# Kernel tuning notes

Measured on AMD Instinct MI355X. Metric: run time of the kernel, lower is better.

## Reference

```python
import jax, jax.numpy as jnp
import numpy as np

THETA = 10000.0
BLOCK_SIZE = 8192  # max_cache_len; T >= BLOCK_SIZE triggers eviction
NEG_INF = -1e30


def _rope_cos_sin(head_dim, seq_len, dtype):
    inv_freq = 1.0 / (THETA ** (jnp.arange(0, head_dim, 2, dtype=jnp.float32) / head_dim))
    freqs = jnp.arange(seq_len, dtype=jnp.float32)[:, None] * inv_freq[None, :]  # (T, hd/2)
    return jnp.cos(freqs).astype(dtype), jnp.sin(freqs).astype(dtype)


def _apply_rope(x, cos, sin):
    # x: (B, T, hd); complex multiply on interleaved pairs, matching torch.view_as_complex
    B, T, hd = x.shape
    xr = x.reshape(B, T, hd // 2, 2)
    x0, x1 = xr[..., 0], xr[..., 1]
    out = jnp.stack([x0 * cos - x1 * sin, x0 * sin + x1 * cos], axis=-1)
    return out.reshape(B, T, hd)


def setup_inputs() -> dict:
    key = jax.random.key(0)
    kx, kk, kq, kv = jax.random.split(key, 4)
    B, T, C, hd = 1, 8192, 1024, 64
    x = jax.random.normal(kx, (B, T, C), dtype=jnp.float32)
    Wk = 0.02 * jax.random.normal(kk, (C, hd), dtype=jnp.float32)
    Wq = 0.02 * jax.random.normal(kq, (C, hd), dtype=jnp.float32)
    Wv = 0.02 * jax.random.normal(kv, (C, hd), dtype=jnp.float32)
    return {"x": x, "Wk": Wk, "Wq": Wq, "Wv": Wv}


def reference(x, Wk, Wq, Wv):
    # Warm-up branch of Head.forward: RoPE QK causal attention + importance-based eviction.
    B, T, C = x.shape
    hd = Wk.shape[1]
    k = x @ Wk  # (B, T, hd)
    q = x @ Wq
    v = x @ Wv
    cos, sin = _rope_cos_sin(hd, T, x.dtype)
    k = _apply_rope(k, cos, sin)
    q = _apply_rope(q, cos, sin)
    scale = hd ** -0.5
    scores = jnp.einsum('btd,bsd->bts', q, k) * scale  # (B, T, T)
    causal = jnp.tril(jnp.ones((T, T), dtype=bool))
    scores = jnp.where(causal[None], scores, NEG_INF)
    wei = jax.nn.softmax(scores, axis=-1)
    out = jnp.einsum('bts,bsd->btd', wei, v)  # (B, T, hd)
    # importance-based KV-cache eviction (T >= BLOCK_SIZE here)
    col_sums = wei.sum(axis=1)  # (B, T)
    evict_id = jnp.argmin(col_sums.reshape(-1))  # flattened argmin, as torch.argmin (B=1)
    keep = jnp.arange(T - 1)
    keep = keep + (keep >= evict_id)  # all indices except evict_id
    importance = jnp.take(wei, keep, axis=1)  # evict row in dim 1: (B, T-1, T)
    cache_k = jnp.take(k, keep, axis=1)       # (B, T-1, hd)
    cache_v = jnp.take(v, keep, axis=1)       # (B, T-1, hd)
    return out, importance, cache_k, cache_v
```

## Files before the change

### kernel.cpp

```cpp
#include <hip/hip_runtime.h>

#define TT 8192
#define CC 1024
#define HD 64
#define TAIL0 (TT - 64)
#define IMP_OFF ((size_t)TT * HD)
#define CK_OFF (IMP_OFF + (size_t)(TT - 1) * TT)
#define CV_OFF (CK_OFF + (size_t)(TT - 1) * HD)

typedef float f32x4 __attribute__((ext_vector_type(4)));
typedef short short8 __attribute__((ext_vector_type(8)));

static __device__ __forceinline__ short f2bf(float f) {
  union { float f; unsigned u; } v; v.f = f;
  unsigned u = v.u;
  unsigned r = (u + 0x7fffu + ((u >> 16) & 1u)) >> 16;
  return (short)r;
}
static __device__ __forceinline__ float bf2f(short h) {
  union { unsigned u; float f; } v;
  v.u = ((unsigned)(unsigned short)h) << 16;
  return v.f;
}
static __device__ __forceinline__ f32x4 mfma16(short8 a, short8 b, f32x4 c) {
  return __builtin_amdgcn_mfma_f32_16x16x32_bf16(a, b, c, 0, 0, 0);
}
static __device__ __forceinline__ void nt_store4(float* p, f32x4 v) {
  __builtin_nontemporal_store(v, (f32x4*)p);
}

__global__ void prep(const float* __restrict__ Wk, const float* __restrict__ Wq,
                     const float* __restrict__ Wv, short* __restrict__ wth,
                     short* __restrict__ wtl, float* __restrict__ colsums,
                     float* __restrict__ ctab, float* __restrict__ stab) {
  const int b = blockIdx.x;
  if (b < 768) {
    const int tid = b * 256 + threadIdx.x;
    const int col = tid >> 10, c = tid & 1023;
    const int m = col >> 6, d = col & 63;
    const float* W = (m == 0) ? Wk : (m == 1) ? Wq : Wv;
    const float w = W[c * HD + d];
    const short h = f2bf(w);
    wth[col * CC + c] = h;
    wtl[col * CC + c] = f2bf(w - bf2f(h));
  } else if (b < 800) {
    const int t = (b - 768) * 256 + threadIdx.x;
    colsums[t] = 0.0f;
  } else {
    const int t = (b - 800) * 256 + threadIdx.x;
    const int row = t >> 5, fi = t & 31;
    const float inv = (float)(1.0 / pow(10000.0, (double)fi / 32.0));
    const float ang = (float)row * inv;
    float sn, cs;
    sincosf(ang, &sn, &cs);
    ctab[t] = cs; stab[t] = sn;
  }
}

__global__ __launch_bounds__(256) void qkv_rope(
    const float* __restrict__ x, const short* __restrict__ wth,
    const short* __restrict__ wtl, const float* __restrict__ ctab,
    const float* __restrict__ stab,
    short* __restrict__ qb, short* __restrict__ kb, short* __restrict__ vt,
    float* __restrict__ kf, float* __restrict__ vf, float* __restrict__ qf) {
  __shared__ short xsh[16][1024];
  __shared__ short xsl[16][1024];
  const int tid = threadIdx.x;
  const int lane = tid & 63, wv = tid >> 6;
  const int g = lane >> 4, lr = lane & 15, g8 = g * 8;
  const int r0 = blockIdx.x * 16;

  for (int i = tid; i < 16 * 128; i += 256) {
    const int row = i >> 7, u = i & 127;
    const float4 a4 = *(const float4*)&x[(size_t)(r0 + row) * CC + u * 8];
    const float4 b4 = *(const float4*)&x[(size_t)(r0 + row) * CC + u * 8 + 4];
    const float xv[8] = {a4.x, a4.y, a4.z, a4.w, b4.x, b4.y, b4.z, b4.w};
    short8 h, l;
#pragma unroll
    for (int t = 0; t < 8; ++t) {
      h[t] = f2bf(xv[t]);
      l[t] = f2bf(xv[t] - bf2f(h[t]));
    }
    const int us = (u ^ (row & 7)) * 8;
    *(short8*)&xsh[row][us] = h;
    *(short8*)&xsl[row][us] = l;
  }
  __syncthreads();

  const int ct0 = wv * 3;
  f32x4 acc[3];
#pragma unroll
  for (int i = 0; i < 3; ++i) acc[i] = (f32x4){0.f, 0.f, 0.f, 0.f};
  for (int kc = 0; kc < 32; ++kc) {
    const int us = ((kc * 4 + g) ^ (lr & 7)) * 8;
    const short8 ah = *(const short8*)&xsh[lr][us];
    const short8 al = *(const short8*)&xsl[lr][us];
    const int k0 = kc * 32 + g8;
#pragma unroll
    for (int t = 0; t < 3; ++t) {
      const int ct = ct0 + t;
      const short8 bh = *(const short8*)&wth[(ct * 16 + lr) * CC + k0];
      const short8 bl = *(const short8*)&wtl[(ct * 16 + lr) * CC + k0];
      acc[t] = mfma16(ah, bh, acc[t]);
      acc[t] = mfma16(al, bh, acc[t]);
      acc[t] = mfma16(ah, bl, acc[t]);
    }
  }
#pragma unroll
  for (int t = 0; t < 3; ++t) {
    const int col = ct0 * 16 + t * 16 + lr;
    const int m = col >> 6, d = col & 63;
#pragma unroll
    for (int r = 0; r < 4; ++r) {
      const int row = r0 + g * 4 + r;
      const float val = acc[t][r];
      if (m == 2) {
        vf[row * HD + d] = val;
        vt[(size_t)d * TT + row] = f2bf(val);
      } else {
        const float partner = __shfl_xor(val, 1);
        const int fi = d >> 1;
        const float cs = ctab[row * 32 + fi];
        const float sn = stab[row * 32 + fi];
        const float res = (d & 1) ? (partner * sn + val * cs)
                                  : (val * cs - partner * sn);
        if (m == 0) { kf[row * HD + d] = res; kb[row * HD + d] = f2bf(res); }
        else        { qf[row * HD + d] = res; qb[row * HD + d] = f2bf(res); }
      }
    }
  }
}

__global__ __launch_bounds__(512) void attn_row(
    const short* __restrict__ qb, const short* __restrict__ kb,
    const short* __restrict__ vt, float* __restrict__ colsums,
    float* __restrict__ outp, float* __restrict__ stash,
    float* __restrict__ linv_g) {
  const int tid = threadIdx.x;
  const int lane = tid & 63, wv = tid >> 6;
  const int g = lane >> 4, lr = lane & 15, g8 = g * 8;
  const int bid = (int)blockIdx.x;
  const int rt = (bid < 256) ? (511 - bid) : (bid - 256);
  const int r0 = rt * 16, rmax = r0 + 15;
  const int nkt = rt + 1;
  const int nktp = (nkt + 1) >> 1;
  float* imp = outp + IMP_OFF;
  const f32x4 z4 = (f32x4){0.f, 0.f, 0.f, 0.f};

  __shared__ float et[8][16][36];
  __shared__ float et2[8][16][36];
  __shared__ float l4[8][16];

  const short8 a0 = *(const short8*)&qb[(r0 + lr) * HD + g8];
  const short8 a1 = *(const short8*)&qb[(r0 + lr) * HD + 32 + g8];

  float lacc[4] = {0.f, 0.f, 0.f, 0.f};
  for (int kt = wv; kt < nkt; kt += 16) {
    const int ktb = kt + 8;
    const bool has1 = (ktb < nkt);
    const int j00 = kt * 16, j01 = ktb * 16;
    const short8 b00 = *(const short8*)&kb[(j00 + lr) * HD + g8];
    const short8 b01 = *(const short8*)&kb[(j00 + lr) * HD + 32 + g8];
    short8 b10, b11;
    if (has1) {
      b10 = *(const short8*)&kb[(j01 + lr) * HD + g8];
      b11 = *(const short8*)&kb[(j01 + lr) * HD + 32 + g8];
    }
    f32x4 sv0 = z4;
    sv0 = mfma16(a0, b00, sv0);
    sv0 = mfma16(a1, b01, sv0);
    f32x4 sv1 = z4;
    if (has1) {
      sv1 = mfma16(a0, b10, sv1);
      sv1 = mfma16(a1, b11, sv1);
    }
    const int jj0 = j00 + lr, jj1 = j01 + lr;
#pragma unroll
    for (int r = 0; r < 4; ++r) {
      const int i = r0 + g * 4 + r;
      if (jj0 <= i) lacc[r] += __expf(sv0[r] * 0.125f);
      if (has1 && jj1 <= i) lacc[r] += __expf(sv1[r] * 0.125f);
    }
  }
#pragma unroll
  for (int r = 0; r < 4; ++r) {
#pragma unroll
    for (int m = 1; m < 16; m <<= 1) lacc[r] += __shfl_xor(lacc[r], m);
  }
  if (lr == 0) {
#pragma unroll
    for (int r = 0; r < 4; ++r) l4[wv][g * 4 + r] = lacc[r];
  }
  __syncthreads();
  float rinv[4];
#pragma unroll
  for (int r = 0; r < 4; ++r) {
    const int row = g * 4 + r;
    float s = 0.f;
#pragma unroll
    for (int w = 0; w < 8; ++w) s += l4[w][row];
    rinv[r] = 1.0f / s;
  }
  if (wv == 0 && lr == 0) {
#pragma unroll
    for (int r = 0; r < 4; ++r) linv_g[r0 + g * 4 + r] = rinv[r];
  }

  f32x4 oacc[4], oacc2[4];
#pragma unroll
  for (int ct = 0; ct < 4; ++ct) { oacc[ct] = z4; oacc2[ct] = z4; }
  const int worow = lane >> 3, wof4 = (lane & 7) * 4;
  for (int kp = wv; kp < nktp; kp += 16) {
    const int kpb = kp + 8;
    const bool has1 = (kpb < nktp);
    const int j0p0 = kp * 32, j0p1 = kpb * 32;
    short8 bv0[4], bv1[4];
#pragma unroll
    for (int ct = 0; ct < 4; ++ct)
      bv0[ct] = *(const short8*)&vt[(size_t)(ct * 16 + lr) * TT + j0p0 + g8];
    if (has1) {
#pragma unroll
      for (int ct = 0; ct < 4; ++ct)
        bv1[ct] = *(const short8*)&vt[(size_t)(ct * 16 + lr) * TT + j0p1 + g8];
    }
#pragma unroll
    for (int c = 0; c < 2; ++c) {
      if (c == 1 && !has1) break;
      const int j0p = c ? j0p1 : j0p0;
      float (*etp)[36] = c ? et2[wv] : et[wv];
#pragma unroll
      for (int h = 0; h < 2; ++h) {
        const int j0 = j0p + h * 16;
        float w4[4] = {0.f, 0.f, 0.f, 0.f};
        if (j0 <= rmax) {
          const short8 b0 = *(const short8*)&kb[(j0 + lr) * HD + g8];
          const short8 b1 = *(const short8*)&kb[(j0 + lr) * HD + 32 + g8];
          f32x4 sv = z4;
          sv = mfma16(a0, b0, sv);
          sv = mfma16(a1, b1, sv);
          const int j = j0 + lr;
#pragma unroll
          for (int r = 0; r < 4; ++r) {
            const int i = r0 + g * 4 + r;
            w4[r] = (j <= i) ? __expf(sv[r] * 0.125f) * rinv[r] : 0.0f;
          }
          float csum = w4[0] + w4[1] + w4[2] + w4[3];
          csum += __shfl_xor(csum, 16);
          csum += __shfl_xor(csum, 32);
          if (lane < 16 && csum > 0.f) atomicAdd(&colsums[j0 + lane], csum);
        }
#pragma unroll
        for (int r = 0; r < 4; ++r) etp[g * 4 + r][h * 16 + lr] = w4[r];
      }
    }
    {
      const float4 e0 = *(const float4*)&et[wv][lr][g8];
      const float4 e1 = *(const float4*)&et[wv][lr][g8 + 4];
      short8 ea;
      ea[0] = f2bf(e0.x); ea[1] = f2bf(e0.y); ea[2] = f2bf(e0.z); ea[3] = f2bf(e0.w);
      ea[4] = f2bf(e1.x); ea[5] = f2bf(e1.y); ea[6] = f2bf(e1.z); ea[7] = f2bf(e1.w);
#pragma unroll
      for (int ct = 0; ct < 4; ++ct) oacc[ct] = mfma16(ea, bv0[ct], oacc[ct]);
    }
    if (has1) {
      const float4 e0 = *(const float4*)&et2[wv][lr][g8];
      const float4 e1 = *(const float4*)&et2[wv][lr][g8 + 4];
      short8 ea;
      ea[0] = f2bf(e0.x); ea[1] = f2bf(e0.y); ea[2] = f2bf(e0.z); ea[3] = f2bf(e0.w);
      ea[4] = f2bf(e1.x); ea[5] = f2bf(e1.y); ea[6] = f2bf(e1.z); ea[7] = f2bf(e1.w);
#pragma unroll
      for (int ct = 0; ct < 4; ++ct) oacc2[ct] = mfma16(ea, bv1[ct], oacc2[ct]);
    }
#pragma unroll
    for (int p = 0; p < 2; ++p) {
      const int row = p * 8 + worow;
      const int i = r0 + row;
      const f32x4 v0 = *(const f32x4*)&et[wv][row][wof4];
      if (i < TT - 1) nt_store4(&imp[(size_t)i * TT + j0p0 + wof4], v0);
      else            *(f32x4*)&stash[j0p0 + wof4] = v0;
      if (has1) {
        const f32x4 v1 = *(const f32x4*)&et2[wv][row][wof4];
        if (i < TT - 1) nt_store4(&imp[(size_t)i * TT + j0p1 + wof4], v1);
        else            *(f32x4*)&stash[j0p1 + wof4] = v1;
      }
    }
  }
  const int zstart = nktp * 32;
  for (int row = 0; row < 16; ++row) {
    const int i = r0 + row;
    if (i < TT - 1) {
      float* dst = &imp[(size_t)i * TT];
      for (int c = zstart + tid * 4; c < TT; c += 2048) nt_store4(&dst[c], z4);
    } else {
      for (int c = zstart + tid * 4; c < TT; c += 2048) *(f32x4*)&stash[c] = z4;
    }
  }
#pragma unroll
  for (int ct = 0; ct < 4; ++ct)
#pragma unroll
    for (int r = 0; r < 4; ++r) oacc[ct][r] += oacc2[ct][r];
  __syncthreads();
  float* cbuf = &et[0][0][0];
#pragma unroll
  for (int step = 4; step >= 1; step >>= 1) {
    if (wv >= step && wv < 2 * step) {
      float* dst = cbuf + (size_t)(wv - step) * 1024;
#pragma unroll
      for (int ct = 0; ct < 4; ++ct)
#pragma unroll
        for (int r = 0; r < 4; ++r)
          dst[(g * 4 + r) * 64 + ct * 16 + lr] = oacc[ct][r];
    }
    __syncthreads();
    if (wv < step) {
      const float* src = cbuf + (size_t)wv * 1024;
#pragma unroll
      for (int ct = 0; ct < 4; ++ct)
#pragma unroll
        for (int r = 0; r < 4; ++r)
          oacc[ct][r] += src[(g * 4 + r) * 64 + ct * 16 + lr];
    }
    __syncthreads();
  }
  if (wv == 0) {
#pragma unroll
    for (int ct = 0; ct < 4; ++ct)
#pragma unroll
      for (int r = 0; r < 4; ++r)
        outp[(size_t)(r0 + g * 4 + r) * HD + ct * 16 + lr] = oacc[ct][r];
  }
}

__global__ __launch_bounds__(256) void tail_exact(
    const float* __restrict__ qf, const float* __restrict__ kf,
    float* __restrict__ l_exact, float* __restrict__ tail_e) {
  const int b = blockIdx.x;
  const int i = TAIL0 + b;
  const int tid = threadIdx.x;
  __shared__ float qs[64];
  __shared__ float ws4[4];
  if (tid < 64) {
    qs[tid] = qf[i * HD + tid];
    if (TAIL0 + tid > i) tail_e[(b << 6) + tid] = 0.0f;
  }
  __syncthreads();
  float part = 0.f;
  for (int j = tid; j <= i; j += 256) {
    const float* kr = &kf[(size_t)j * HD];
    float dot = 0.f;
#pragma unroll
    for (int d = 0; d < 64; ++d) dot += qs[d] * kr[d];
    const float e = expf(dot * 0.125f);
    part += e;
    if (j >= TAIL0) tail_e[(b << 6) + (j - TAIL0)] = e;
  }
#pragma unroll
  for (int m = 1; m < 64; m <<= 1) part += __shfl_xor(part, m);
  if ((tid & 63) == 0) ws4[tid >> 6] = part;
  __syncthreads();
  if (tid == 0) l_exact[b] = ws4[0] + ws4[1] + ws4[2] + ws4[3];
}

__global__ void argmin_k(const float* __restrict__ colsums,
                         const float* __restrict__ l_exact,
                         const float* __restrict__ tail_e,
                         int* __restrict__ evict) {
  __shared__ float sv[4];
  __shared__ int si[4];
  const int tid = threadIdx.x, lane = tid & 63, wv = tid >> 6;
  float best = 3.4e38f; int bi = TT;
  for (int j = tid; j < TT; j += 256) {
    float v;
    if (j >= TAIL0) {
      const int jc = j - TAIL0;
      v = 0.f;
      for (int b = jc; b < 64; ++b) v += tail_e[(b << 6) + jc] / l_exact[b];
    } else {
      v = colsums[j];
    }
    if (v < best) { best = v; bi = j; }
  }
#pragma unroll
  for (int m = 1; m < 64; m <<= 1) {
    const float ov = __shfl_xor(best, m);
    const int oi = __shfl_xor(bi, m);
    if (ov < best || (ov == best && oi < bi)) { best = ov; bi = oi; }
  }
  if (lane == 0) { sv[wv] = best; si[wv] = bi; }
  __syncthreads();
  if (tid == 0) {
    for (int w = 1; w < 4; ++w)
      if (sv[w] < best || (sv[w] == best && si[w] < bi)) { best = sv[w]; bi = si[w]; }
    evict[0] = bi;
  }
}

__global__ __launch_bounds__(256) void fix_cache(
    const float* __restrict__ qf, const float* __restrict__ kf,
    const float* __restrict__ vf, const float* __restrict__ linv,
    const float* __restrict__ stash, const int* __restrict__ evict,
    float* __restrict__ outp) {
  const int bid = (int)blockIdx.x;
  const int tid = threadIdx.x;
  const int eid = evict[0];
  if (bid < 512) {
    float* imp = outp + IMP_OFF;
    __shared__ float qs[64];
    for (int dst = eid + bid; dst < TT - 1; dst += 512) {
      const int src = dst + 1;
      if (src == TT - 1) {
        for (int c = tid; c < TT / 4; c += 256)
          ((f32x4*)&imp[(size_t)dst * TT])[c] = ((const f32x4*)stash)[c];
      } else {
        if (tid < 64) qs[tid] = qf[src * HD + tid];
        __syncthreads();
        const float rinv = linv[src];
        for (int j = tid; j < TT; j += 256) {
          float w = 0.f;
          if (j <= src) {
            const float* kr = &kf[(size_t)j * HD];
            float dot = 0.f;
#pragma unroll
            for (int d = 0; d < 64; ++d) dot += qs[d] * kr[d];
            w = expf(dot * 0.125f) * rinv;
          }
          imp[(size_t)dst * TT + j] = w;
        }
        __syncthreads();
      }
    }
  } else {
    const int t = (bid - 512) * 256 + tid;
    const int per = (TT - 1) * (HD / 4);
    if (t >= 2 * per) return;
    const int m = t / per;
    const int rem = t - m * per;
    const int r = rem >> 4, c4 = rem & 15;
    const int src = r + (r >= eid);
    const float* sp = m ? vf : kf;
    const f32x4 val = *(const f32x4*)&sp[src * HD + c4 * 4];
    float* dst = outp + (m ? CV_OFF : CK_OFF);
    nt_store4(&dst[r * HD + c4 * 4], val);
  }
}

extern "C" void kernel_launch(void* const* d_in, const int* in_sizes, int n_in,
                              void* d_out, int out_size, void* d_ws, size_t ws_size,
                              hipStream_t stream) {
  const float* x  = (const float*)d_in[0];
  const float* Wk = (const float*)d_in[1];
  const float* Wq = (const float*)d_in[2];
  const float* Wv = (const float*)d_in[3];
  float* outp = (float*)d_out;
  char* ws = (char*)d_ws;
  short* qb      = (short*)(ws);
  short* kb      = (short*)(ws + (1u << 20));
  short* vt      = (short*)(ws + (2u << 20));
  float* kf      = (float*)(ws + (3u << 20));
  float* vf      = (float*)(ws + (5u << 20));
  float* qf      = (float*)(ws + (7u << 20));
  float* linv    = (float*)(ws + (9u << 20));
  int*   evict   = (int*)  (ws + (9u << 20) + (64u << 10));
  float* colsums = (float*)(ws + (9u << 20) + (384u << 10));
  short* wth     = (short*)(ws + (9u << 20) + (448u << 10));
  short* wtl     = (short*)(ws + (9u << 20) + (832u << 10));
  float* tail_e  = (float*)(ws + (9u << 20) + (1280u << 10));
  float* l_exact = (float*)(ws + (9u << 20) + (1344u << 10));
  float* stash   = (float*)(ws + (9u << 20) + (1408u << 10));
  float* ctab    = (float*)(ws + (12u << 20));
  float* stab    = (float*)(ws + (13u << 20));

  prep<<<1824, 256, 0, stream>>>(Wk, Wq, Wv, wth, wtl, colsums, ctab, stab);
  qkv_rope<<<512, 256, 0, stream>>>(x, wth, wtl, ctab, stab, qb, kb, vt, kf, vf, qf);
  attn_row<<<512, 512, 0, stream>>>(qb, kb, vt, colsums, outp, stash, linv);
  tail_exact<<<64, 256, 0, stream>>>(qf, kf, l_exact, tail_e);
  argmin_k<<<1, 256, 0, stream>>>(colsums, l_exact, tail_e, evict);
  fix_cache<<<1536, 256, 0, stream>>>(qf, kf, vf, linv, stash, evict, outp);
}
```

Measured before the change: 264.2 us.

## Merge zero-fill into main loop and widen importance row stores to 512B segments

Each wave now processes four consecutive 32-column chunks across all 256 column chunks of the row tile. It writes zeros for chunks past the causal limit inside the same loop, so the separate zero-fill pass is gone. The per-wave LDS staging buffer is widened to 128 columns, so each importance row is written as a contiguous 512-byte segment instead of 128-byte pieces. The second accumulator and the dual-chunk interleave are removed, which may reduce ILP for the MFMA and V loads, and the larger shared buffer may lower occupancy.

```diff
diff --git a/kernel.cpp b/kernel.cpp
--- a/kernel.cpp
+++ b/kernel.cpp
@@ -143,12 +143,10 @@
   const int rt = (bid < 256) ? (511 - bid) : (bid - 256);
   const int r0 = rt * 16, rmax = r0 + 15;
   const int nkt = rt + 1;
-  const int nktp = (nkt + 1) >> 1;
   float* imp = outp + IMP_OFF;
   const f32x4 z4 = (f32x4){0.f, 0.f, 0.f, 0.f};
 
-  __shared__ float et[8][16][36];
-  __shared__ float et2[8][16][36];
+  __shared__ float et[8][16][132];
   __shared__ float l4[8][16];
 
   const short8 a0 = *(const short8*)&qb[(r0 + lr) * HD + g8];
@@ -206,28 +204,23 @@
     for (int r = 0; r < 4; ++r) linv_g[r0 + g * 4 + r] = rinv[r];
   }
 
-  f32x4 oacc[4], oacc2[4];
-#pragma unroll
-  for (int ct = 0; ct < 4; ++ct) { oacc[ct] = z4; oacc2[ct] = z4; }
-  const int worow = lane >> 3, wof4 = (lane & 7) * 4;
-  for (int kp = wv; kp < nktp; kp += 16) {
-    const int kpb = kp + 8;
-    const bool has1 = (kpb < nktp);
-    const int j0p0 = kp * 32, j0p1 = kpb * 32;
-    short8 bv0[4], bv1[4];
-#pragma unroll
-    for (int ct = 0; ct < 4; ++ct)
-      bv0[ct] = *(const short8*)&vt[(size_t)(ct * 16 + lr) * TT + j0p0 + g8];
-    if (has1) {
-#pragma unroll
-      for (int ct = 0; ct < 4; ++ct)
-        bv1[ct] = *(const short8*)&vt[(size_t)(ct * 16 + lr) * TT + j0p1 + g8];
-    }
-#pragma unroll
-    for (int c = 0; c < 2; ++c) {
-      if (c == 1 && !has1) break;
-      const int j0p = c ? j0p1 : j0p0;
-      float (*etp)[36] = c ? et2[wv] : et[wv];
+  f32x4 oacc[4];
+#pragma unroll
+  for (int ct = 0; ct < 4; ++ct) oacc[ct] = z4;
+  const int colslot4 = (lane & 31) * 4;
+  const int srow2 = lane >> 5;
+  for (int kp0 = wv * 4; kp0 < 256; kp0 += 32) {
+#pragma unroll
+    for (int kpi = 0; kpi < 4; ++kpi) {
+      const int kp = kp0 + kpi;
+      const int j0p = kp * 32;
+      const bool act = (j0p <= rmax);
+      short8 bv[4];
+      if (act) {
+#pragma unroll
+        for (int ct = 0; ct < 4; ++ct)
+          bv[ct] = *(const short8*)&vt[(size_t)(ct * 16 + lr) * TT + j0p + g8];
+      }
 #pragma unroll
       for (int h = 0; h < 2; ++h) {
         const int j0 = j0p + h * 16;
@@ -250,55 +243,30 @@
           if (lane < 16 && csum > 0.f) atomicAdd(&colsums[j0 + lane], csum);
         }
 #pragma unroll
-        for (int r = 0; r < 4; ++r) etp[g * 4 + r][h * 16 + lr] = w4[r];
+        for (int r = 0; r < 4; ++r)
+          et[wv][g * 4 + r][kpi * 32 + h * 16 + lr] = w4[r];
       }
-    }
-    {
-      const float4 e0 = *(const float4*)&et[wv][lr][g8];
-      const float4 e1 = *(const float4*)&et[wv][lr][g8 + 4];
-      short8 ea;
-      ea[0] = f2bf(e0.x); ea[1] = f2bf(e0.y); ea[2] = f2bf(e0.z); ea[3] = f2bf(e0.w);
-      ea[4] = f2bf(e1.x); ea[5] = f2bf(e1.y); ea[6] = f2bf(e1.z); ea[7] = f2bf(e1.w);
-#pragma unroll
-      for (int ct = 0; ct < 4; ++ct) oacc[ct] = mfma16(ea, bv0[ct], oacc[ct]);
-    }
-    if (has1) {
-      const float4 e0 = *(const float4*)&et2[wv][lr][g8];
-      const float4 e1 = *(const float4*)&et2[wv][lr][g8 + 4];
-      short8 ea;
-      ea[0] = f2bf(e0.x); ea[1] = f2bf(e0.y); ea[2] = f2bf(e0.z); ea[3] = f2bf(e0.w);
-      ea[4] = f2bf(e1.x); ea[5] = f2bf(e1.y); ea[6] = f2bf(e1.z); ea[7] = f2bf(e1.w);
-#pragma unroll
-      for (int ct = 0; ct < 4; ++ct) oacc2[ct] = mfma16(ea, bv1[ct], oacc2[ct]);
-    }
-#pragma unroll
-    for (int p = 0; p < 2; ++p) {
-      const int row = p * 8 + worow;
+      if (act) {
+        const float4 e0 = *(const float4*)&et[wv][lr][kpi * 32 + g8];
+        const float4 e1 = *(const float4*)&et[wv][lr][kpi * 32 + g8 + 4];
+        short8 ea;
+        ea[0] = f2bf(e0.x); ea[1] = f2bf(e0.y); ea[2] = f2bf(e0.z); ea[3] = f2bf(e0.w);
+        ea[4] = f2bf(e1.x); ea[5] = f2bf(e1.y); ea[6] = f2bf(e1.z); ea[7] = f2bf(e1.w);
+#pragma unroll
+        for (int ct = 0; ct < 4; ++ct) oacc[ct] = mfma16(ea, bv[ct], oacc[ct]);
+      }
+    }
+    const int j00 = kp0 * 32;
+#pragma unroll
+    for (int p = 0; p < 8; ++p) {
+      const int row = p * 2 + srow2;
       const int i = r0 + row;
-      const f32x4 v0 = *(const f32x4*)&et[wv][row][wof4];
-      if (i < TT - 1) nt_store4(&imp[(size_t)i * TT + j0p0 + wof4], v0);
-      else            *(f32x4*)&stash[j0p0 + wof4] = v0;
-      if (has1) {
-        const f32x4 v1 = *(const f32x4*)&et2[wv][row][wof4];
-        if (i < TT - 1) nt_store4(&imp[(size_t)i * TT + j0p1 + wof4], v1);
-        else            *(f32x4*)&stash[j0p1 + wof4] = v1;
-      }
-    }
-  }
-  const int zstart = nktp * 32;
-  for (int row = 0; row < 16; ++row) {
-    const int i = r0 + row;
-    if (i < TT - 1) {
-      float* dst = &imp[(size_t)i * TT];
-      for (int c = zstart + tid * 4; c < TT; c += 2048) nt_store4(&dst[c], z4);
-    } else {
-      for (int c = zstart + tid * 4; c < TT; c += 2048) *(f32x4*)&stash[c] = z4;
-    }
-  }
-#pragma unroll
-  for (int ct = 0; ct < 4; ++ct)
-#pragma unroll
-    for (int r = 0; r < 4; ++r) oacc[ct][r] += oacc2[ct][r];
+      const f32x4 v = *(const f32x4*)&et[wv][row][colslot4];
+      if (i < TT - 1) nt_store4(&imp[(size_t)i * TT + j00 + colslot4], v);
+      else            *(f32x4*)&stash[j00 + colslot4] = v;
+    }
+  }
+
   __syncthreads();
   float* cbuf = &et[0][0][0];
 #pragma unroll
```

New measurement: 265.8 us. Within noise of the previous version (+0.6%).
